# Kernel optimization log

Hardware: AMD Instinct MI355X
Metric: run time of the kernel (lower is better)

## Reference

```python
import jax, jax.numpy as jnp
import numpy as np

MASK_RATIO = 0.1


def _masked_channels(c, mask_ratio):
    # Faithful to the original: np.linspace float membership test against int i
    end = c * (1.0 - mask_ratio)
    stride = int(c * mask_ratio)
    mask = np.linspace(0.0, end, stride)
    sel = [i for i in range(c) if i in mask]
    return np.asarray(sel, dtype=np.int32)


def setup_inputs() -> dict:
    key = jax.random.key(0)
    input1 = jax.random.normal(key, (4, 100, 512, 512), dtype=jnp.float32)
    return {"input1": input1}


def reference(input1) -> jnp.ndarray:
    b, c, h, w = input1.shape
    sel = _masked_channels(c, MASK_RATIO)  # static channel index set
    x = input1.reshape(b, c, h * w)  # [N, L, D]
    # Original fills each selected channel with fresh torch.randn([N, D]);
    # one fused fill: noise [N, n_sel, D], single scatter over channel axis.
    noise = jax.random.normal(jax.random.key(1), (b, sel.shape[0], h * w), dtype=x.dtype)
    x = x.at[:, sel, :].set(noise)
    return x.reshape(b, c, h, w)
```

## Files before the change

### kernel.cpp

```cpp
#include <hip/hip_runtime.h>
#include <stdint.h>


__device__ __forceinline__ uint32_t rotl32(uint32_t v, int r) {
    return (v << r) | (v >> (32 - r));
}

__device__ __forceinline__ void threefry2x32_key01(uint32_t x0, uint32_t x1,
                                                   uint32_t& o0, uint32_t& o1) {
    const uint32_t ks0 = 0u;
    const uint32_t ks1 = 1u;
    const uint32_t ks2 = 0x1BD11BDAu ^ ks0 ^ ks1;
    x0 += ks0; x1 += ks1;
#define TF_R(r) { x0 += x1; x1 = rotl32(x1, (r)); x1 ^= x0; }
    TF_R(13) TF_R(15) TF_R(26) TF_R(6)
    x0 += ks1; x1 += ks2 + 1u;
    TF_R(17) TF_R(29) TF_R(16) TF_R(24)
    x0 += ks2; x1 += ks0 + 2u;
    TF_R(13) TF_R(15) TF_R(26) TF_R(6)
    x0 += ks0; x1 += ks1 + 3u;
    TF_R(17) TF_R(29) TF_R(16) TF_R(24)
    x0 += ks1; x1 += ks2 + 4u;
    TF_R(13) TF_R(15) TF_R(26) TF_R(6)
    x0 += ks2; x1 += ks0 + 5u;
#undef TF_R
    o0 = x0; o1 = x1;
}

__device__ __forceinline__ float erfinv_xla_f32(float x) {
    float w = -log1pf(-x * x);
    float p;
    if (w < 5.0f) {
        w = w - 2.5f;
        p = 2.81022636e-08f;
        p = fmaf(p, w, 3.43273939e-07f);
        p = fmaf(p, w, -3.5233877e-06f);
        p = fmaf(p, w, -4.39150654e-06f);
        p = fmaf(p, w, 0.00021858087f);
        p = fmaf(p, w, -0.00125372503f);
        p = fmaf(p, w, -0.00417768164f);
        p = fmaf(p, w, 0.246640727f);
        p = fmaf(p, w, 1.50140941f);
    } else {
        w = sqrtf(w) - 3.0f;
        p = -0.000200214257f;
        p = fmaf(p, w, 0.000100950558f);
        p = fmaf(p, w, 0.00134934322f);
        p = fmaf(p, w, -0.00367342844f);
        p = fmaf(p, w, 0.00573950773f);
        p = fmaf(p, w, -0.0076224613f);
        p = fmaf(p, w, 0.00943887047f);
        p = fmaf(p, w, 1.00167406f);
        p = fmaf(p, w, 2.83297682f);
    }
    return p * x;
}

__device__ __forceinline__ float bits_to_normal(uint32_t bits) {
    float f = __uint_as_float((bits >> 9) | 0x3F800000u) - 1.0f;
    const float lo = __uint_as_float(0xBF7FFFFFu);
    float u = f * 2.0f + lo;
    u = fmaxf(lo, u);
    const float sqrt2 = __uint_as_float(0x3FB504F3u);
    return sqrt2 * erfinv_xla_f32(u);
}

constexpr uint32_t CH4    = 65536u;
constexpr uint32_t TOTAL4 = 4u * 100u * CH4;

__global__ __launch_bounds__(256) void random_masking_kernel(
        const float4* __restrict__ in, float4* __restrict__ out) {
    uint32_t stride = gridDim.x * blockDim.x;
    for (uint32_t i = blockIdx.x * blockDim.x + threadIdx.x; i < TOTAL4; i += stride) {
        uint32_t cb = i >> 16;
        uint32_t c  = cb % 100u;
        if (c % 10u != 0u) {
            out[i] = in[i];
        } else {
            uint32_t b = cb / 100u;
            uint32_t s = c / 10u;
            uint32_t j = ((b * 10u + s) << 18) | ((i & 65535u) << 2);
            float4 o;
            float* po = reinterpret_cast<float*>(&o);
#pragma unroll
            for (int e = 0; e < 4; ++e) {
                uint32_t y0, y1;
                threefry2x32_key01(0u, j + (uint32_t)e, y0, y1);
                po[e] = bits_to_normal(y0 ^ y1);
            }
            out[i] = o;
        }
    }
}

extern "C" void kernel_launch(void* const* d_in, const int* in_sizes, int n_in,
                              void* d_out, int out_size, void* d_ws, size_t ws_size,
                              hipStream_t stream) {
    const float4* in = reinterpret_cast<const float4*>(d_in[0]);
    float4* out = reinterpret_cast<float4*>(d_out);
    random_masking_kernel<<<2048, 256, 0, stream>>>(in, out);
}
```

Measured before the change: 160.8 us.

## Tile grid per channel with uniform block branches and nontemporal loads/stores

Replaces the grid-stride loop with one block per 2048-float4 tile of a single channel. Each block therefore takes a uniform copy or noise path with no per-element divergence, and the per-element channel arithmetic goes away. The copy path issues 8 independent nontemporal loads before its stores to raise memory-level parallelism, and all stores are nontemporal to avoid polluting the cache. The cost is many more blocks and a hardcoded shape.

```diff
diff --git a/kernel.cpp b/kernel.cpp
--- a/kernel.cpp
+++ b/kernel.cpp
@@ -1,6 +1,8 @@
 #include <hip/hip_runtime.h>
 #include <stdint.h>
 
+
+typedef float f32x4 __attribute__((ext_vector_type(4)));
 
 __device__ __forceinline__ uint32_t rotl32(uint32_t v, int r) {
     return (v << r) | (v >> (32 - r));
@@ -65,30 +67,42 @@
     return sqrt2 * erfinv_xla_f32(u);
 }
 
-constexpr uint32_t CH4    = 65536u;
-constexpr uint32_t TOTAL4 = 4u * 100u * CH4;
+constexpr uint32_t TILE_SHIFT = 11;
+constexpr uint32_t TILES_PER_CH = 32;
+constexpr uint32_t NBLOCKS = 400u * TILES_PER_CH;
 
 __global__ __launch_bounds__(256) void random_masking_kernel(
-        const float4* __restrict__ in, float4* __restrict__ out) {
-    uint32_t stride = gridDim.x * blockDim.x;
-    for (uint32_t i = blockIdx.x * blockDim.x + threadIdx.x; i < TOTAL4; i += stride) {
-        uint32_t cb = i >> 16;
-        uint32_t c  = cb % 100u;
-        if (c % 10u != 0u) {
-            out[i] = in[i];
-        } else {
-            uint32_t b = cb / 100u;
-            uint32_t s = c / 10u;
-            uint32_t j = ((b * 10u + s) << 18) | ((i & 65535u) << 2);
-            float4 o;
-            float* po = reinterpret_cast<float*>(&o);
+        const f32x4* __restrict__ in, f32x4* __restrict__ out) {
+    const uint32_t bid  = blockIdx.x;
+    const uint32_t cb   = bid >> 5;
+    const uint32_t tile = bid & (TILES_PER_CH - 1);
+    const uint32_t c    = cb % 100u;
+    const uint32_t base = (cb << 16) + (tile << TILE_SHIFT) + threadIdx.x;
+
+    if (c % 10u != 0u) {
+        f32x4 v[8];
+#pragma unroll
+        for (int k = 0; k < 8; ++k)
+            v[k] = __builtin_nontemporal_load(in + base + k * 256);
+#pragma unroll
+        for (int k = 0; k < 8; ++k)
+            __builtin_nontemporal_store(v[k], out + base + k * 256);
+    } else {
+        const uint32_t b = cb / 100u;
+        const uint32_t s = c / 10u;
+        const uint32_t jch = (b * 10u + s) << 18;
+        const uint32_t fch = (tile << TILE_SHIFT) + threadIdx.x;
+#pragma unroll
+        for (int k = 0; k < 8; ++k) {
+            const uint32_t j = jch + ((fch + k * 256) << 2);
+            f32x4 o;
 #pragma unroll
             for (int e = 0; e < 4; ++e) {
                 uint32_t y0, y1;
                 threefry2x32_key01(0u, j + (uint32_t)e, y0, y1);
-                po[e] = bits_to_normal(y0 ^ y1);
+                o[e] = bits_to_normal(y0 ^ y1);
             }
-            out[i] = o;
+            __builtin_nontemporal_store(o, out + base + k * 256);
         }
     }
 }
@@ -96,7 +110,7 @@
 extern "C" void kernel_launch(void* const* d_in, const int* in_sizes, int n_in,
                               void* d_out, int out_size, void* d_ws, size_t ws_size,
                               hipStream_t stream) {
-    const float4* in = reinterpret_cast<const float4*>(d_in[0]);
-    float4* out = reinterpret_cast<float4*>(d_out);
-    random_masking_kernel<<<2048, 256, 0, stream>>>(in, out);
+    const f32x4* in = reinterpret_cast<const f32x4*>(d_in[0]);
+    f32x4* out = reinterpret_cast<f32x4*>(d_out);
+    random_masking_kernel<<<NBLOCKS, 256, 0, stream>>>(in, out);
 }
```

Measured after the change: 151.5 us. 5.8% less time.
